# Performance work log

Hardware: AMD Instinct MI355X
Metric: run time of the kernel (lower is better)

Reference implementation:

```python
import jax, jax.numpy as jnp
import numpy as np

EPS = 1e-5
GROUPS = 32


def _groupnorm(x, gamma, beta):
    B, C, H, W = x.shape
    xr = x.reshape(B, GROUPS, C // GROUPS, H, W)
    mu = xr.mean(axis=(2, 3, 4), keepdims=True)
    var = xr.var(axis=(2, 3, 4), keepdims=True)
    xn = ((xr - mu) * jax.lax.rsqrt(var + EPS)).reshape(B, C, H, W)
    return xn * gamma[None, :, None, None] + beta[None, :, None, None]


def _conv1x1(x, w, b):
    # x: [B,C,H,W], w: [Cout,Cin], b: [Cout]
    return jnp.einsum('bchw,oc->bohw', x, w) + b[None, :, None, None]


def setup_inputs() -> dict:
    key = jax.random.key(0)
    ks = jax.random.split(key, 11)
    B, C, H, W = 4, 64, 64, 64
    s = 0.05  # weight scale for well-conditioned softmax
    inp = {
        'x': jax.random.normal(ks[0], (B, C, H, W), jnp.float32),
        'gn_gamma': jnp.ones((C,), jnp.float32),
        'gn_beta': jnp.zeros((C,), jnp.float32),
        'wq': jax.random.normal(ks[1], (C, C), jnp.float32) * s,
        'bq': jnp.zeros((C,), jnp.float32),
        'wk': jax.random.normal(ks[2], (C, C), jnp.float32) * s,
        'bk': jnp.zeros((C,), jnp.float32),
        'wv': jax.random.normal(ks[3], (C, C), jnp.float32) * s,
        'bv': jnp.zeros((C,), jnp.float32),
        'wp': jax.random.normal(ks[4], (C, C), jnp.float32) * s,
        'bp': jnp.zeros((C,), jnp.float32),
    }
    return inp


def reference(x, gn_gamma, gn_beta, wq, bq, wk, bk, wv, bv, wp, bp):
    B, C, H, W = x.shape
    h = _groupnorm(x, gn_gamma, gn_beta)
    q = _conv1x1(h, wq, bq)
    k = _conv1x1(h, wk, bk)
    v = _conv1x1(h, wv, bv)
    # scores over all spatial positions: [B,H,W,H,W]
    scale = 1.0 / jnp.sqrt(jnp.asarray(C, x.dtype))
    w = jnp.einsum('bchw,bcHW->bhwHW', q, k) * scale
    w = jax.nn.softmax(w.reshape(B, H, W, H * W), axis=-1).reshape(B, H, W, H, W)
    h = jnp.einsum('bhwHW,bcHW->bchw', w, v)
    h = _conv1x1(h, wp, bp)
    return x + h
```

## Files before the change

kernel.cpp:

```cpp
#include <hip/hip_runtime.h>
#include <stdint.h>

#define Bn 4
#define Cn 64
#define Sn 4096
#define Gn 32

typedef float v4f __attribute__((ext_vector_type(4)));
typedef short v8s __attribute__((ext_vector_type(8)));

#define MFMA16(a,b,c) __builtin_amdgcn_mfma_f32_16x16x32_bf16((a),(b),(c),0,0,0)

__device__ __forceinline__ float bf2f(uint16_t u){
  union { uint32_t i; float f; } x; x.i = ((uint32_t)u) << 16; return x.f;
}
__device__ __forceinline__ uint16_t f2bf(float f){
  union { float f; uint32_t i; } x; x.f = f;
  uint32_t r = x.i + 0x7fffu + ((x.i >> 16) & 1u);
  return (uint16_t)(r >> 16);
}
__device__ __forceinline__ v8s pack8(float4 a, float4 b){
  v8s r;
  r[0]=(short)f2bf(a.x); r[1]=(short)f2bf(a.y); r[2]=(short)f2bf(a.z); r[3]=(short)f2bf(a.w);
  r[4]=(short)f2bf(b.x); r[5]=(short)f2bf(b.y); r[6]=(short)f2bf(b.z); r[7]=(short)f2bf(b.w);
  return r;
}

__global__ __launch_bounds__(256) void gn_stats(const float* __restrict__ x,
                                                float* __restrict__ stats)
{
  const int tid = threadIdx.x;
  const float* base = x + (size_t)blockIdx.x * 8192;
  float sum = 0.f, sq = 0.f;
  #pragma unroll
  for (int i = 0; i < 8; ++i) {
    float4 v = *(const float4*)(base + ((i << 8) + tid)*4);
    sum += v.x + v.y + v.z + v.w;
    sq  += v.x*v.x + v.y*v.y + v.z*v.z + v.w*v.w;
  }
  #pragma unroll
  for (int off = 1; off < 64; off <<= 1) {
    sum += __shfl_xor(sum, off);
    sq  += __shfl_xor(sq, off);
  }
  __shared__ float red[8];
  const int w = tid >> 6;
  if ((tid & 63) == 0) { red[w] = sum; red[4+w] = sq; }
  __syncthreads();
  if (tid == 0) {
    float s = red[0]+red[1]+red[2]+red[3];
    float q = red[4]+red[5]+red[6]+red[7];
    float mean = s * (1.f/8192.f);
    float var  = q * (1.f/8192.f) - mean*mean;
    stats[blockIdx.x]       = mean;
    stats[128 + blockIdx.x] = rsqrtf(fmaxf(var, 0.f) + 1e-5f);
  }
}

__global__ __launch_bounds__(256) void gn_qkv(
    const float* __restrict__ xg, const float* __restrict__ gamma,
    const float* __restrict__ beta,
    const float* __restrict__ wq, const float* __restrict__ bq,
    const float* __restrict__ wk, const float* __restrict__ bk,
    const float* __restrict__ wv, const float* __restrict__ bv,
    const float* __restrict__ stats,
    uint16_t* __restrict__ Qg, uint16_t* __restrict__ Kg, uint16_t* __restrict__ Vg)
{
  __shared__ uint16_t Hs[64*72];
  const int tid  = threadIdx.x;
  const int w    = tid >> 6;
  const int lane = tid & 63;
  const int l15  = lane & 15;
  const int quad = lane >> 4;
  const int b      = blockIdx.x >> 6;
  const int s_base = (blockIdx.x & 63) << 6;

  {
    const int c = lane;
    const int g = c >> 1;
    const float mean = stats[b*Gn + g];
    const float rstd = stats[128 + b*Gn + g];
    const float ga = gamma[c], be = beta[c];
    const float* xr = xg + ((size_t)b*Cn + c)*Sn + s_base + (w << 4);
    #pragma unroll
    for (int j = 0; j < 16; j += 4) {
      float4 v = *(const float4*)(xr + j);
      const int srow = (w << 4) + j;
      Hs[(srow+0)*72 + c] = f2bf((v.x - mean)*rstd*ga + be);
      Hs[(srow+1)*72 + c] = f2bf((v.y - mean)*rstd*ga + be);
      Hs[(srow+2)*72 + c] = f2bf((v.z - mean)*rstd*ga + be);
      Hs[(srow+3)*72 + c] = f2bf((v.w - mean)*rstd*ga + be);
    }
  }
  __syncthreads();

  const int brow = (w << 4) + l15;
  v8s bh0 = *(const v8s*)(Hs + brow*72 + (quad << 3));
  v8s bh1 = *(const v8s*)(Hs + brow*72 + 32 + (quad << 3));

  const float* Ws[3] = {wq, wk, wv};
  const float* Bs[3] = {bq, bk, bv};
  #pragma unroll
  for (int ot = 0; ot < 12; ++ot) {
    const int wsel = ot >> 2;
    const int o16  = (ot & 3) << 4;
    const float* Wr = Ws[wsel] + (o16 + l15)*64 + (quad << 3);
    v8s a0 = pack8(*(const float4*)(Wr),      *(const float4*)(Wr + 4));
    v8s a1 = pack8(*(const float4*)(Wr + 32), *(const float4*)(Wr + 36));
    v4f d = (v4f){0.f,0.f,0.f,0.f};
    d = MFMA16(a0, bh0, d);
    d = MFMA16(a1, bh1, d);
    const int s = s_base + (w << 4) + l15;
    #pragma unroll
    for (int r = 0; r < 4; ++r) {
      const int o = o16 + (quad << 2) + r;
      const float val = d[r] + Bs[wsel][o];
      if (wsel == 0)      Qg[((size_t)b*Sn + s)*64 + o] = f2bf(val);
      else if (wsel == 1) Kg[((size_t)b*Sn + s)*64 + o] = f2bf(val);
      else                Vg[((size_t)b*Cn + o)*Sn + s] = f2bf(val);
    }
  }
}

__global__ __launch_bounds__(256) void attn_split(
    const uint16_t* __restrict__ Qg, const uint16_t* __restrict__ Kg,
    const uint16_t* __restrict__ Vg,
    uint16_t* __restrict__ Opart, float* __restrict__ lpart)
{
  __shared__ uint16_t Qs[64*72];
  __shared__ uint16_t Ks[64*72];
  __shared__ uint16_t Vs[64*72];
  __shared__ uint16_t Ps[4][16*72];

  const int tid  = threadIdx.x;
  const int w    = tid >> 6;
  const int lane = tid & 63;
  const int l15  = lane & 15;
  const int quad = lane >> 4;
  const int bx    = blockIdx.x;
  const int split = bx & 3;
  const int qt    = (bx >> 2) & 63;
  const int b     = bx >> 8;
  const int i_base = qt << 6;
  const int j0     = split << 10;

  const uint16_t* Qb = Qg + ((size_t)b*Sn + i_base)*64;
  const uint16_t* Kb = Kg + (size_t)b*Sn*64;
  const uint16_t* Vb = Vg + (size_t)b*Cn*Sn;

  #pragma unroll
  for (int i = 0; i < 2; ++i) {
    const int e   = ((i << 8) + tid) << 3;
    const int row = e >> 6, col = e & 63;
    *(v8s*)(Qs + row*72 + col) = *(const v8s*)(Qb + e);
  }

  float lsum[4];
  v4f o_acc[4];
  #pragma unroll
  for (int r = 0; r < 4; ++r) lsum[r] = 0.f;
  #pragma unroll
  for (int n = 0; n < 4; ++n) o_acc[n] = (v4f){0.f,0.f,0.f,0.f};

  __syncthreads();

  const int arow = (w << 4) + l15;
  v8s aq0 = *(const v8s*)(Qs + arow*72 + (quad << 3));
  v8s aq1 = *(const v8s*)(Qs + arow*72 + 32 + (quad << 3));

  const float SC = 0.18033688011112042f;

  for (int kt = 0; kt < 16; ++kt) {
    const int jb = j0 + (kt << 6);
    __syncthreads();
    #pragma unroll
    for (int i = 0; i < 2; ++i) {
      const int e   = ((i << 8) + tid) << 3;
      const int row = e >> 6, col = e & 63;
      *(v8s*)(Ks + row*72 + col) = *(const v8s*)(Kb + jb*64 + e);
      *(v8s*)(Vs + row*72 + col) = *(const v8s*)(Vb + (size_t)row*Sn + jb + col);
    }
    __syncthreads();

    v4f s[4];
    #pragma unroll
    for (int n = 0; n < 4; ++n) {
      const uint16_t* kr = Ks + ((n << 4) + l15)*72;
      v8s b0 = *(const v8s*)(kr + (quad << 3));
      v8s b1 = *(const v8s*)(kr + 32 + (quad << 3));
      v4f t = (v4f){0.f,0.f,0.f,0.f};
      t = MFMA16(aq0, b0, t);
      t = MFMA16(aq1, b1, t);
      s[n] = t;
    }

    uint16_t* Pw = Ps[w];
    #pragma unroll
    for (int n = 0; n < 4; ++n) {
      #pragma unroll
      for (int r = 0; r < 4; ++r) {
        const float pv = __builtin_amdgcn_exp2f(s[n][r]*SC);
        lsum[r] += pv;
        Pw[((quad << 2) + r)*72 + (n << 4) + l15] = f2bf(pv);
      }
    }

    __asm__ volatile("" ::: "memory");

    v8s ap0 = *(const v8s*)(Pw + l15*72 + (quad << 3));
    v8s ap1 = *(const v8s*)(Pw + l15*72 + 32 + (quad << 3));

    #pragma unroll
    for (int n = 0; n < 4; ++n) {
      const uint16_t* vrp = Vs + ((n << 4) + l15)*72;
      v8s b0 = *(const v8s*)(vrp + (quad << 3));
      v8s b1 = *(const v8s*)(vrp + 32 + (quad << 3));
      v4f o = o_acc[n];
      o = MFMA16(ap0, b0, o);
      o = MFMA16(ap1, b1, o);
      o_acc[n] = o;
    }
  }

  #pragma unroll
  for (int r = 0; r < 4; ++r) {
    lsum[r] += __shfl_xor(lsum[r], 1);
    lsum[r] += __shfl_xor(lsum[r], 2);
    lsum[r] += __shfl_xor(lsum[r], 4);
    lsum[r] += __shfl_xor(lsum[r], 8);
  }

  uint16_t* Ob = Opart + (size_t)bx*4096 + (w << 4)*64;
  float*    lp = lpart + bx*64 + (w << 4);
  #pragma unroll
  for (int n = 0; n < 4; ++n)
    #pragma unroll
    for (int r = 0; r < 4; ++r)
      Ob[((quad << 2) + r)*64 + (n << 4) + l15] = f2bf(o_acc[n][r]);
  if (l15 == 0) {
    #pragma unroll
    for (int r = 0; r < 4; ++r) lp[(quad << 2) + r] = lsum[r];
  }
}

__global__ __launch_bounds__(256) void proj_res(
    const uint16_t* __restrict__ Opart, const float* __restrict__ lpart,
    const float* __restrict__ wp, const float* __restrict__ bp,
    const float* __restrict__ xg, float* __restrict__ out)
{
  __shared__ uint16_t As[64*72];
  const int tid  = threadIdx.x;
  const int w    = tid >> 6;
  const int lane = tid & 63;
  const int l15  = lane & 15;
  const int quad = lane >> 4;
  const int bx   = blockIdx.x;
  const int b      = bx >> 6;
  const int s_base = (bx & 63) << 6;

  const uint16_t* po = Opart + (size_t)bx*4*4096;
  const float*    pl = lpart + bx*4*64;

  #pragma unroll
  for (int i = 0; i < 2; ++i) {
    const int e   = ((i << 8) + tid) << 3;
    const int row = e >> 6, col = e & 63;
    const float linv = 1.f / (pl[row] + pl[64+row] + pl[128+row] + pl[192+row]);
    float acc[8] = {0,0,0,0,0,0,0,0};
    #pragma unroll
    for (int sp = 0; sp < 4; ++sp) {
      v8s o = *(const v8s*)(po + sp*4096 + e);
      #pragma unroll
      for (int j = 0; j < 8; ++j) acc[j] += bf2f((uint16_t)o[j]);
    }
    v8s a;
    #pragma unroll
    for (int j = 0; j < 8; ++j) a[j] = (short)f2bf(acc[j]*linv);
    *(v8s*)(As + row*72 + col) = a;
  }
  __syncthreads();

  const int arow = (w << 4) + l15;
  v8s ba0 = *(const v8s*)(As + arow*72 + (quad << 3));
  v8s ba1 = *(const v8s*)(As + arow*72 + 32 + (quad << 3));

  #pragma unroll
  for (int mt = 0; mt < 4; ++mt) {
    const float* Wr = wp + ((mt << 4) + l15)*64 + (quad << 3);
    v8s a0 = pack8(*(const float4*)(Wr),      *(const float4*)(Wr + 4));
    v8s a1 = pack8(*(const float4*)(Wr + 32), *(const float4*)(Wr + 36));
    v4f d = (v4f){0.f,0.f,0.f,0.f};
    d = MFMA16(a0, ba0, d);
    d = MFMA16(a1, ba1, d);
    const int s = s_base + (w << 4) + l15;
    #pragma unroll
    for (int r = 0; r < 4; ++r) {
      const int o = (mt << 4) + (quad << 2) + r;
      const size_t idx = ((size_t)b*Cn + o)*Sn + s;
      out[idx] = d[r] + bp[o] + xg[idx];
    }
  }
}

extern "C" void kernel_launch(void* const* d_in, const int* in_sizes, int n_in,
                              void* d_out, int out_size, void* d_ws, size_t ws_size,
                              hipStream_t stream)
{
  const float* x     = (const float*)d_in[0];
  const float* gamma = (const float*)d_in[1];
  const float* beta  = (const float*)d_in[2];
  const float* wq    = (const float*)d_in[3];
  const float* bq    = (const float*)d_in[4];
  const float* wk    = (const float*)d_in[5];
  const float* bk    = (const float*)d_in[6];
  const float* wv    = (const float*)d_in[7];
  const float* bv    = (const float*)d_in[8];
  const float* wp    = (const float*)d_in[9];
  const float* bp    = (const float*)d_in[10];

  float*    stats = (float*)d_ws;
  uint16_t* Qg    = (uint16_t*)d_ws + 1024;
  uint16_t* Kg    = Qg + (size_t)Bn*Sn*Cn;
  uint16_t* Vg    = Kg + (size_t)Bn*Sn*Cn;
  uint16_t* Opart = Vg + (size_t)Bn*Sn*Cn;
  float*    lpart = (float*)(Opart + (size_t)1024*4096);
  float*    outp  = (float*)d_out;

  gn_stats  <<<128, 256, 0, stream>>>(x, stats);
  gn_qkv    <<<256, 256, 0, stream>>>(x, gamma, beta, wq, bq, wk, bk, wv, bv,
                                      stats, Qg, Kg, Vg);
  attn_split<<<1024, 256, 0, stream>>>(Qg, Kg, Vg, Opart, lpart);
  proj_res  <<<256, 256, 0, stream>>>(Opart, lpart, wp, bp, x, outp);
}
```

Baseline: 135.1 us.

## Register-prefetch K/V tiles in attention and split QKV/projection work across more blocks

The attention kernel now loads the next K/V tile into registers before computing on the current one, then writes it to shared memory after a barrier, so global load latency overlaps the MFMA work. Q fragments are read straight from global memory into registers instead of going through shared memory. The QKV and output-projection kernels are repartitioned into 1024 blocks, each handling 16 spatial positions with the output tiles spread across warps, and Q/K stores are vectorised. This raises parallelism in the small kernels, at the cost of more register pressure in attention and redundant weight loads per block.

```diff
diff --git a/kernel.cpp b/kernel.cpp
--- a/kernel.cpp
+++ b/kernel.cpp
@@ -8,6 +8,7 @@
 
 typedef float v4f __attribute__((ext_vector_type(4)));
 typedef short v8s __attribute__((ext_vector_type(8)));
+typedef short v4s __attribute__((ext_vector_type(4)));
 
 #define MFMA16(a,b,c) __builtin_amdgcn_mfma_f32_16x16x32_bf16((a),(b),(c),0,0,0)
 
@@ -66,14 +67,14 @@
     const float* __restrict__ stats,
     uint16_t* __restrict__ Qg, uint16_t* __restrict__ Kg, uint16_t* __restrict__ Vg)
 {
-  __shared__ uint16_t Hs[64*72];
+  __shared__ uint16_t Hs[16*72];
   const int tid  = threadIdx.x;
   const int w    = tid >> 6;
   const int lane = tid & 63;
   const int l15  = lane & 15;
   const int quad = lane >> 4;
-  const int b      = blockIdx.x >> 6;
-  const int s_base = (blockIdx.x & 63) << 6;
+  const int b      = blockIdx.x >> 8;
+  const int s_base = (blockIdx.x & 255) << 4;
 
   {
     const int c = lane;
@@ -81,43 +82,45 @@
     const float mean = stats[b*Gn + g];
     const float rstd = stats[128 + b*Gn + g];
     const float ga = gamma[c], be = beta[c];
-    const float* xr = xg + ((size_t)b*Cn + c)*Sn + s_base + (w << 4);
-    #pragma unroll
-    for (int j = 0; j < 16; j += 4) {
-      float4 v = *(const float4*)(xr + j);
-      const int srow = (w << 4) + j;
-      Hs[(srow+0)*72 + c] = f2bf((v.x - mean)*rstd*ga + be);
-      Hs[(srow+1)*72 + c] = f2bf((v.y - mean)*rstd*ga + be);
-      Hs[(srow+2)*72 + c] = f2bf((v.z - mean)*rstd*ga + be);
-      Hs[(srow+3)*72 + c] = f2bf((v.w - mean)*rstd*ga + be);
-    }
+    float4 v = *(const float4*)(xg + ((size_t)b*Cn + c)*Sn + s_base + (w << 2));
+    const int r0 = w << 2;
+    Hs[(r0+0)*72 + c] = f2bf((v.x - mean)*rstd*ga + be);
+    Hs[(r0+1)*72 + c] = f2bf((v.y - mean)*rstd*ga + be);
+    Hs[(r0+2)*72 + c] = f2bf((v.z - mean)*rstd*ga + be);
+    Hs[(r0+3)*72 + c] = f2bf((v.w - mean)*rstd*ga + be);
   }
   __syncthreads();
 
-  const int brow = (w << 4) + l15;
-  v8s bh0 = *(const v8s*)(Hs + brow*72 + (quad << 3));
-  v8s bh1 = *(const v8s*)(Hs + brow*72 + 32 + (quad << 3));
-
-  const float* Ws[3] = {wq, wk, wv};
-  const float* Bs[3] = {bq, bk, bv};
-  #pragma unroll
-  for (int ot = 0; ot < 12; ++ot) {
+  v8s bh0 = *(const v8s*)(Hs + l15*72 + (quad << 3));
+  v8s bh1 = *(const v8s*)(Hs + l15*72 + 32 + (quad << 3));
+
+  #pragma unroll
+  for (int t = 0; t < 3; ++t) {
+    const int ot   = w*3 + t;
     const int wsel = ot >> 2;
     const int o16  = (ot & 3) << 4;
-    const float* Wr = Ws[wsel] + (o16 + l15)*64 + (quad << 3);
+    const float* Wsel = (wsel == 0) ? wq : (wsel == 1) ? wk : wv;
+    const float* Bsel = (wsel == 0) ? bq : (wsel == 1) ? bk : bv;
+    const float* Wr = Wsel + (o16 + l15)*64 + (quad << 3);
     v8s a0 = pack8(*(const float4*)(Wr),      *(const float4*)(Wr + 4));
     v8s a1 = pack8(*(const float4*)(Wr + 32), *(const float4*)(Wr + 36));
     v4f d = (v4f){0.f,0.f,0.f,0.f};
     d = MFMA16(a0, bh0, d);
     d = MFMA16(a1, bh1, d);
-    const int s = s_base + (w << 4) + l15;
-    #pragma unroll
-    for (int r = 0; r < 4; ++r) {
-      const int o = o16 + (quad << 2) + r;
-      const float val = d[r] + Bs[wsel][o];
-      if (wsel == 0)      Qg[((size_t)b*Sn + s)*64 + o] = f2bf(val);
-      else if (wsel == 1) Kg[((size_t)b*Sn + s)*64 + o] = f2bf(val);
-      else                Vg[((size_t)b*Cn + o)*Sn + s] = f2bf(val);
+    const int s = s_base + l15;
+    if (wsel <= 1) {
+      v4s qv;
+      #pragma unroll
+      for (int r = 0; r < 4; ++r)
+        qv[r] = (short)f2bf(d[r] + Bsel[o16 + (quad << 2) + r]);
+      uint16_t* dst = (wsel == 0 ? Qg : Kg) + ((size_t)b*Sn + s)*64 + o16 + (quad << 2);
+      *(v4s*)dst = qv;
+    } else {
+      #pragma unroll
+      for (int r = 0; r < 4; ++r) {
+        const int o = o16 + (quad << 2) + r;
+        Vg[((size_t)b*Cn + o)*Sn + s] = f2bf(d[r] + Bsel[o]);
+      }
     }
   }
 }
@@ -127,7 +130,6 @@
     const uint16_t* __restrict__ Vg,
     uint16_t* __restrict__ Opart, float* __restrict__ lpart)
 {
-  __shared__ uint16_t Qs[64*72];
   __shared__ uint16_t Ks[64*72];
   __shared__ uint16_t Vs[64*72];
   __shared__ uint16_t Ps[4][16*72];
@@ -148,12 +150,17 @@
   const uint16_t* Kb = Kg + (size_t)b*Sn*64;
   const uint16_t* Vb = Vg + (size_t)b*Cn*Sn;
 
-  #pragma unroll
-  for (int i = 0; i < 2; ++i) {
-    const int e   = ((i << 8) + tid) << 3;
-    const int row = e >> 6, col = e & 63;
-    *(v8s*)(Qs + row*72 + col) = *(const v8s*)(Qb + e);
-  }
+  const int arow = (w << 4) + l15;
+  v8s aq0 = *(const v8s*)(Qb + arow*64 + (quad << 3));
+  v8s aq1 = *(const v8s*)(Qb + arow*64 + 32 + (quad << 3));
+
+  const int e0 = tid << 3,        r0 = e0 >> 6, c0 = e0 & 63;
+  const int e1 = (256 + tid) << 3, r1 = e1 >> 6, c1 = e1 & 63;
+
+  *(v8s*)(Ks + r0*72 + c0) = *(const v8s*)(Kb + j0*64 + e0);
+  *(v8s*)(Ks + r1*72 + c1) = *(const v8s*)(Kb + j0*64 + e1);
+  *(v8s*)(Vs + r0*72 + c0) = *(const v8s*)(Vb + (size_t)r0*Sn + j0 + c0);
+  *(v8s*)(Vs + r1*72 + c1) = *(const v8s*)(Vb + (size_t)r1*Sn + j0 + c1);
 
   float lsum[4];
   v4f o_acc[4];
@@ -164,23 +171,17 @@
 
   __syncthreads();
 
-  const int arow = (w << 4) + l15;
-  v8s aq0 = *(const v8s*)(Qs + arow*72 + (quad << 3));
-  v8s aq1 = *(const v8s*)(Qs + arow*72 + 32 + (quad << 3));
-
   const float SC = 0.18033688011112042f;
 
   for (int kt = 0; kt < 16; ++kt) {
-    const int jb = j0 + (kt << 6);
-    __syncthreads();
-    #pragma unroll
-    for (int i = 0; i < 2; ++i) {
-      const int e   = ((i << 8) + tid) << 3;
-      const int row = e >> 6, col = e & 63;
-      *(v8s*)(Ks + row*72 + col) = *(const v8s*)(Kb + jb*64 + e);
-      *(v8s*)(Vs + row*72 + col) = *(const v8s*)(Vb + (size_t)row*Sn + jb + col);
-    }
-    __syncthreads();
+    v8s kp0, kp1, vp0, vp1;
+    if (kt < 15) {
+      const int jb = j0 + ((kt + 1) << 6);
+      kp0 = *(const v8s*)(Kb + jb*64 + e0);
+      kp1 = *(const v8s*)(Kb + jb*64 + e1);
+      vp0 = *(const v8s*)(Vb + (size_t)r0*Sn + jb + c0);
+      vp1 = *(const v8s*)(Vb + (size_t)r1*Sn + jb + c1);
+    }
 
     v4f s[4];
     #pragma unroll
@@ -220,6 +221,15 @@
       o = MFMA16(ap1, b1, o);
       o_acc[n] = o;
     }
+
+    __syncthreads();
+    if (kt < 15) {
+      *(v8s*)(Ks + r0*72 + c0) = kp0;
+      *(v8s*)(Ks + r1*72 + c1) = kp1;
+      *(v8s*)(Vs + r0*72 + c0) = vp0;
+      *(v8s*)(Vs + r1*72 + c1) = vp1;
+    }
+    __syncthreads();
   }
 
   #pragma unroll
@@ -248,57 +258,53 @@
     const float* __restrict__ wp, const float* __restrict__ bp,
     const float* __restrict__ xg, float* __restrict__ out)
 {
-  __shared__ uint16_t As[64*72];
+  __shared__ uint16_t As[16*72];
   const int tid  = threadIdx.x;
   const int w    = tid >> 6;
   const int lane = tid & 63;
   const int l15  = lane & 15;
   const int quad = lane >> 4;
-  const int bx   = blockIdx.x;
-  const int b      = bx >> 6;
-  const int s_base = (bx & 63) << 6;
-
-  const uint16_t* po = Opart + (size_t)bx*4*4096;
-  const float*    pl = lpart + bx*4*64;
-
-  #pragma unroll
-  for (int i = 0; i < 2; ++i) {
-    const int e   = ((i << 8) + tid) << 3;
-    const int row = e >> 6, col = e & 63;
+  const int b      = blockIdx.x >> 8;
+  const int st     = blockIdx.x & 255;
+  const int qt     = st >> 2;
+  const int sub    = st & 3;
+  const int s_base = st << 4;
+
+  const uint16_t* po = Opart + (size_t)((b*64 + qt)*4)*4096 + (sub << 4)*64;
+  const float*    pl = lpart + ((b*64 + qt)*4)*64 + (sub << 4);
+
+  {
+    const int e = tid << 2, row = tid >> 4, col = (tid & 15) << 2;
     const float linv = 1.f / (pl[row] + pl[64+row] + pl[128+row] + pl[192+row]);
-    float acc[8] = {0,0,0,0,0,0,0,0};
+    float acc[4] = {0.f,0.f,0.f,0.f};
     #pragma unroll
     for (int sp = 0; sp < 4; ++sp) {
-      v8s o = *(const v8s*)(po + sp*4096 + e);
+      v4s o = *(const v4s*)(po + sp*4096 + e);
       #pragma unroll
-      for (int j = 0; j < 8; ++j) acc[j] += bf2f((uint16_t)o[j]);
-    }
-    v8s a;
-    #pragma unroll
-    for (int j = 0; j < 8; ++j) a[j] = (short)f2bf(acc[j]*linv);
-    *(v8s*)(As + row*72 + col) = a;
+      for (int j = 0; j < 4; ++j) acc[j] += bf2f((uint16_t)o[j]);
+    }
+    v4s a;
+    #pragma unroll
+    for (int j = 0; j < 4; ++j) a[j] = (short)f2bf(acc[j]*linv);
+    *(v4s*)(As + row*72 + col) = a;
   }
   __syncthreads();
 
-  const int arow = (w << 4) + l15;
-  v8s ba0 = *(const v8s*)(As + arow*72 + (quad << 3));
-  v8s ba1 = *(const v8s*)(As + arow*72 + 32 + (quad << 3));
-
-  #pragma unroll
-  for (int mt = 0; mt < 4; ++mt) {
-    const float* Wr = wp + ((mt << 4) + l15)*64 + (quad << 3);
-    v8s a0 = pack8(*(const float4*)(Wr),      *(const float4*)(Wr + 4));
-    v8s a1 = pack8(*(const float4*)(Wr + 32), *(const float4*)(Wr + 36));
-    v4f d = (v4f){0.f,0.f,0.f,0.f};
-    d = MFMA16(a0, ba0, d);
-    d = MFMA16(a1, ba1, d);
-    const int s = s_base + (w << 4) + l15;
-    #pragma unroll
-    for (int r = 0; r < 4; ++r) {
-      const int o = (mt << 4) + (quad << 2) + r;
-      const size_t idx = ((size_t)b*Cn + o)*Sn + s;
-      out[idx] = d[r] + bp[o] + xg[idx];
-    }
+  v8s ba0 = *(const v8s*)(As + l15*72 + (quad << 3));
+  v8s ba1 = *(const v8s*)(As + l15*72 + 32 + (quad << 3));
+
+  const float* Wr = wp + ((w << 4) + l15)*64 + (quad << 3);
+  v8s a0 = pack8(*(const float4*)(Wr),      *(const float4*)(Wr + 4));
+  v8s a1 = pack8(*(const float4*)(Wr + 32), *(const float4*)(Wr + 36));
+  v4f d = (v4f){0.f,0.f,0.f,0.f};
+  d = MFMA16(a0, ba0, d);
+  d = MFMA16(a1, ba1, d);
+  const int s = s_base + l15;
+  #pragma unroll
+  for (int r = 0; r < 4; ++r) {
+    const int o = (w << 4) + (quad << 2) + r;
+    const size_t idx = ((size_t)b*Cn + o)*Sn + s;
+    out[idx] = d[r] + bp[o] + xg[idx];
   }
 }
 
@@ -327,8 +333,8 @@
   float*    outp  = (float*)d_out;
 
   gn_stats  <<<128, 256, 0, stream>>>(x, stats);
-  gn_qkv    <<<256, 256, 0, stream>>>(x, gamma, beta, wq, bq, wk, bk, wv, bv,
-                                      stats, Qg, Kg, Vg);
+  gn_qkv    <<<1024, 256, 0, stream>>>(x, gamma, beta, wq, bq, wk, bk, wv, bv,
+                                       stats, Qg, Kg, Vg);
   attn_split<<<1024, 256, 0, stream>>>(Qg, Kg, Vg, Opart, lpart);
-  proj_res  <<<256, 256, 0, stream>>>(Opart, lpart, wp, bp, x, outp);
-}
+  proj_res  <<<1024, 256, 0, stream>>>(Opart, lpart, wp, bp, x, outp);
+}
```

Measured after the change: 132.1 us. 1.02x faster.
